# Kernel optimization log

Measured on AMD Instinct MI355X. Metric: run time of the kernel, lower is better.

Reference implementation:

```python
import jax, jax.numpy as jnp
import numpy as np

N, E, IN, H, C = 100_000, 1_600_000, 128, 4, 32  # nodes, edges, in_dim, heads, per-head channels
HC = H * C
SLOPE = 0.2  # negative_slope


def setup_inputs() -> dict:
    key = jax.random.key(0)
    ks = jax.random.split(key, 20)
    rn = lambda k, shape, s=0.05: jax.random.normal(k, shape, jnp.float32) * s
    inp = {
        'x': rn(ks[0], (N, IN), 1.0),
        'edge_index': jax.random.randint(ks[1], (2, E), 0, N),
    }
    for i in range(3):
        din = IN if i == 0 else HC
        inp[f'W{i}'] = rn(ks[2 + 4 * i], (din, HC))
        inp[f'as{i}'] = rn(ks[3 + 4 * i], (H, C))
        inp[f'ad{i}'] = rn(ks[4 + 4 * i], (H, C))
        inp[f'b{i}'] = jnp.zeros((HC,), jnp.float32)
    inp['llW'] = rn(ks[14], (HC, HC))
    inp['llb'] = jnp.zeros((HC,), jnp.float32)
    inp['opW'] = rn(ks[15], (3 * HC, C))  # concat_dim=384 -> out_dim=32
    inp['opb'] = jnp.zeros((C,), jnp.float32)
    return inp


def gat_layer(h, src, dst, W, a_s, a_d, b):
    # PyG GATConv with concat=True, add_self_loops=False, edge_dim=None, eval-mode dropout
    xh = (h @ W).reshape(-1, H, C)                        # [N,H,C]
    e_src = (xh * a_s).sum(-1)                            # [N,H]
    e_dst = (xh * a_d).sum(-1)                            # [N,H]
    e = jax.nn.leaky_relu(e_src[src] + e_dst[dst], SLOPE)  # [E,H]
    emax = jax.ops.segment_max(e, dst, num_segments=N)    # segment softmax over dst
    ee = jnp.exp(e - emax[dst])
    denom = jax.ops.segment_sum(ee, dst, num_segments=N)
    alpha = ee / denom[dst]                               # [E,H]
    out = jax.ops.segment_sum(xh[src] * alpha[:, :, None], dst, num_segments=N)  # [N,H,C]
    return out.reshape(-1, HC) + b


def reference(x, edge_index, W0, as0, ad0, b0, W1, as1, ad1, b1, W2, as2, ad2, b2, llW, llb, opW, opb):
    src, dst = edge_index[0], edge_index[1]
    # layer 0 (no residual at layer 0)
    h0 = gat_layer(x, src, dst, W0, as0, ad0, b0)
    # layer 1: residual
    h1 = gat_layer(h0, src, dst, W1, as1, ad1, b1) + h0
    # layer 2: residual through last_linear
    h2 = gat_layer(h1, src, dst, W2, as2, ad2, b2) + (h1 @ llW + llb)
    # encoder head: concat hidden list, project
    h = jnp.concatenate([h0, h1, h2], axis=-1)  # [N, 384]
    return h @ opW + opb                         # [N, 32]
```

## Files before the change

### kernel.cpp

```cpp
#include <hip/hip_runtime.h>
#include <hip/hip_bf16.h>

#define NN  100000
#define NE  1600000
#define NH4 400000
#define NHC 12800000
#define NBLK 391
#define SC_CHUNK 2048
#define SC_NCHUNK ((NE + SC_CHUNK - 1) / SC_CHUNK)

typedef __attribute__((ext_vector_type(8))) short bf16x8;
typedef __attribute__((ext_vector_type(4))) float f32x4;

__device__ __forceinline__ ushort f2bf(float f) {
  uint u = __float_as_uint(f);
  u += 0x7fff + ((u >> 16) & 1);
  return (ushort)(u >> 16);
}
__device__ __forceinline__ uint pack2(float a, float b) {
  return (uint)f2bf(a) | ((uint)f2bf(b) << 16);
}
__device__ __forceinline__ float blo(uint u) { return __uint_as_float(u << 16); }
__device__ __forceinline__ float bhi(uint u) { return __uint_as_float(u & 0xffff0000u); }

template <bool ABF16>
__global__ __launch_bounds__(256) void gemm128_k(const void* __restrict__ Av,
                                                 const float* __restrict__ W,
                                                 ushort* __restrict__ out,
                                                 const float* __restrict__ bias1,
                                                 const float* __restrict__ bias2) {
  __shared__ uint As[64 * 64];
  __shared__ uint Wt[128 * 64];
  const int tid = threadIdx.x;
  const int row0 = blockIdx.x * 64;

  if constexpr (ABF16) {
    const uint4* __restrict__ Ag = (const uint4*)((const uint*)Av + (size_t)row0 * 64);
#pragma unroll
    for (int i = 0; i < 4; i++) {
      const int idx = tid + 256 * i;
      const int r = idx >> 4, c4 = idx & 15;
      uint4 v = make_uint4(0u, 0u, 0u, 0u);
      if (row0 + r < NN) v = Ag[idx];
      const uint off = (uint)(r * 64 + c4 * 4) ^ (uint)((r & 7) << 2);
      *(uint4*)&As[off] = v;
    }
  } else {
    const float4* __restrict__ Ag = (const float4*)((const float*)Av + (size_t)row0 * 128);
#pragma unroll
    for (int i = 0; i < 8; i++) {
      const int idx = tid + 256 * i;
      const int r = idx >> 5, k4 = idx & 31;
      float4 a = make_float4(0.f, 0.f, 0.f, 0.f);
      if (row0 + r < NN) a = Ag[idx];
      uint2 p;
      p.x = pack2(a.x, a.y);
      p.y = pack2(a.z, a.w);
      const uint off = (uint)(r * 64 + k4 * 2) ^ (uint)((r & 7) << 2);
      *(uint2*)&As[off] = p;
    }
  }
  {
#pragma unroll
    for (int i = 0; i < 8; i++) {
      const int cid = tid + 256 * i;
      const int n = cid & 127;
      const int k8 = cid >> 7;
      float v[8];
#pragma unroll
      for (int j = 0; j < 8; j++) v[j] = W[(size_t)(k8 * 8 + j) * 128 + n];
      uint4 p;
      p.x = pack2(v[0], v[1]);
      p.y = pack2(v[2], v[3]);
      p.z = pack2(v[4], v[5]);
      p.w = pack2(v[6], v[7]);
      const uint off = (uint)(n * 64 + k8 * 4) ^ (uint)((n & 7) << 2);
      *(uint4*)&Wt[off] = p;
    }
  }
  __syncthreads();

  const int w = tid >> 6, l = tid & 63;
  const int lrow = l & 15;
  const int lku = (l >> 4) * 4;

  bf16x8 afrag[4];
#pragma unroll
  for (int kc = 0; kc < 4; kc++) {
    const int r = w * 16 + lrow;
    const uint off = (uint)(r * 64 + lku + kc * 16) ^ (uint)((r & 7) << 2);
    afrag[kc] = *(const bf16x8*)&As[off];
  }

#pragma unroll
  for (int nt = 0; nt < 8; nt++) {
    const int n = nt * 16 + lrow;
    f32x4 acc = {0.f, 0.f, 0.f, 0.f};
#pragma unroll
    for (int kc = 0; kc < 4; kc++) {
      const uint off = (uint)(n * 64 + lku + kc * 16) ^ (uint)((n & 7) << 2);
      const bf16x8 bfrag = *(const bf16x8*)&Wt[off];
      acc = __builtin_amdgcn_mfma_f32_16x16x32_bf16(afrag[kc], bfrag, acc, 0, 0, 0);
    }
    const int col = n;
    float badd = 0.f;
    if (bias1) badd += bias1[col];
    if (bias2) badd += bias2[col];
#pragma unroll
    for (int reg = 0; reg < 4; reg++) {
      const int r = row0 + w * 16 + (l >> 4) * 4 + reg;
      if (r < NN) out[(size_t)r * 128 + col] = f2bf(acc[reg] + badd);
    }
  }
}

__global__ __launch_bounds__(256) void attn_coef_k(const uint* __restrict__ xbf,
                                                   const float* __restrict__ as_,
                                                   const float* __restrict__ ad_,
                                                   float* __restrict__ es,
                                                   float* __restrict__ ed) {
  const int idx = blockIdx.x * 256 + threadIdx.x;
  if (idx >= NH4) return;
  const int h = idx & 3;
  const int ab = h * 32;
  const uint* row = xbf + (size_t)(idx >> 2) * 64 + h * 16;
  float s = 0.f, d = 0.f;
#pragma unroll
  for (int i = 0; i < 16; i += 4) {
    const uint4 v = *(const uint4*)(row + i);
#define UNP(u, k)                                                        \
    {                                                                    \
      const float lo = blo(u), hi = bhi(u);                              \
      s = fmaf(lo, as_[ab + (k)], fmaf(hi, as_[ab + (k) + 1], s));       \
      d = fmaf(lo, ad_[ab + (k)], fmaf(hi, ad_[ab + (k) + 1], d));       \
    }
    UNP(v.x, 2 * i) UNP(v.y, 2 * i + 2) UNP(v.z, 2 * i + 4) UNP(v.w, 2 * i + 6)
#undef UNP
  }
  es[idx] = s;
  ed[idx] = d;
}

__global__ __launch_bounds__(256) void hist_k(const int* __restrict__ dst, int* __restrict__ counts) {
  const int g = blockIdx.x & 7;
  const int chunk = blockIdx.x >> 3;
  const int lo = g * (NN / 8);
  const int hi = lo + (NN / 8);
  const int e0 = chunk * SC_CHUNK;
  const int e1 = (e0 + SC_CHUNK < NE) ? e0 + SC_CHUNK : NE;
  for (int i = e0 + threadIdx.x; i < e1; i += 256) {
    const int d = dst[i];
    if (d >= lo && d < hi) atomicAdd(&counts[d], 1);
  }
}

__global__ __launch_bounds__(256) void scan_blk_k(const int* __restrict__ counts,
                                                  int* __restrict__ row_start,
                                                  int* __restrict__ blocksum) {
  __shared__ int sm[256];
  const int t = threadIdx.x;
  const int i = blockIdx.x * 256 + t;
  const int c = (i < NN) ? counts[i] : 0;
  sm[t] = c;
  __syncthreads();
#pragma unroll
  for (int off = 1; off < 256; off <<= 1) {
    const int v = (t >= off) ? sm[t - off] : 0;
    __syncthreads();
    sm[t] += v;
    __syncthreads();
  }
  if (i < NN) row_start[i] = sm[t] - c;
  if (t == 255) blocksum[blockIdx.x] = sm[255];
}

__global__ __launch_bounds__(512) void scan_top_k(const int* __restrict__ blocksum,
                                                  int* __restrict__ blockoff) {
  __shared__ int sm[512];
  const int t = threadIdx.x;
  const int c = (t < NBLK) ? blocksum[t] : 0;
  sm[t] = c;
  __syncthreads();
#pragma unroll
  for (int off = 1; off < 512; off <<= 1) {
    const int v = (t >= off) ? sm[t - off] : 0;
    __syncthreads();
    sm[t] += v;
    __syncthreads();
  }
  if (t < NBLK) blockoff[t] = sm[t] - c;
}

__global__ __launch_bounds__(256) void scan_fix_k(int* __restrict__ row_start,
                                                  const int* __restrict__ blockoff,
                                                  int* __restrict__ cursor) {
  const int i = blockIdx.x * 256 + threadIdx.x;
  if (i < NN) {
    const int v = row_start[i] + blockoff[blockIdx.x];
    row_start[i] = v;
    cursor[i] = v;
  }
  if (i == 0) row_start[NN] = NE;
}

__global__ __launch_bounds__(256) void scatter_k(const int* __restrict__ src,
                                                 const int* __restrict__ dst,
                                                 int* __restrict__ cursor,
                                                 int* __restrict__ csr_src) {
  const int g = blockIdx.x & 7;
  const int chunk = blockIdx.x >> 3;
  const int lo = g * (NN / 8);
  const int hi = lo + (NN / 8);
  const int e0 = chunk * SC_CHUNK;
  const int e1 = (e0 + SC_CHUNK < NE) ? e0 + SC_CHUNK : NE;
  for (int i = e0 + threadIdx.x; i < e1; i += 256) {
    const int d = dst[i];
    if (d >= lo && d < hi) {
      const int pos = atomicAdd(&cursor[d], 1);
      csr_src[pos] = src[i];
    }
  }
}

#define EDGE_BODY(sv)                                                      \
  {                                                                        \
    const int s_ = (sv);                                                   \
    float v_ = es[s_ * 4 + h] + edh;                                       \
    v_ = v_ > 0.f ? v_ : 0.2f * v_;                                        \
    const float w_ = __expf(v_);                                           \
    const uint m_ = xbf[(size_t)s_ * 64 + l];                              \
    den += w_;                                                             \
    ax = fmaf(w_, blo(m_), ax);                                            \
    ay = fmaf(w_, bhi(m_), ay);                                            \
  }

__global__ __launch_bounds__(256) void gat_agg_k(const int* __restrict__ row_start,
                                                 const int* __restrict__ csr_src,
                                                 const float* __restrict__ es,
                                                 const float* __restrict__ ed,
                                                 const uint* __restrict__ xbf,
                                                 const ushort* __restrict__ base,
                                                 const float* __restrict__ bias,
                                                 ushort* __restrict__ out) {
  const int wid = (blockIdx.x * 256 + threadIdx.x) >> 6;
  if (wid >= NN) return;
  const int l = threadIdx.x & 63;
  const int h = l >> 4;
  const float edh = ed[wid * 4 + h];
  const int beg = row_start[wid], end = row_start[wid + 1];
  float ax = 0.f, ay = 0.f, den = 0.f;
  int i = beg;
  for (; i + 8 <= end; i += 8) {
    const int s0 = csr_src[i],     s1 = csr_src[i + 1];
    const int s2 = csr_src[i + 2], s3 = csr_src[i + 3];
    const int s4 = csr_src[i + 4], s5 = csr_src[i + 5];
    const int s6 = csr_src[i + 6], s7 = csr_src[i + 7];
    EDGE_BODY(s0) EDGE_BODY(s1) EDGE_BODY(s2) EDGE_BODY(s3)
    EDGE_BODY(s4) EDGE_BODY(s5) EDGE_BODY(s6) EDGE_BODY(s7)
  }
  for (; i + 4 <= end; i += 4) {
    const int s0 = csr_src[i],     s1 = csr_src[i + 1];
    const int s2 = csr_src[i + 2], s3 = csr_src[i + 3];
    EDGE_BODY(s0) EDGE_BODY(s1) EDGE_BODY(s2) EDGE_BODY(s3)
  }
  for (; i < end; i++) EDGE_BODY(csr_src[i]);

  const float inv = den > 0.f ? 1.f / den : 0.f;
  float rx = ax * inv, ry = ay * inv;
  const size_t o = (size_t)wid * 64 + l;
  if (base) {
    const uint b = ((const uint*)base)[o];
    rx += blo(b); ry += bhi(b);
  }
  if (bias) { rx += bias[l * 2]; ry += bias[l * 2 + 1]; }
  ((uint*)out)[o] = pack2(rx, ry);
}

__global__ __launch_bounds__(256) void out_proj_k(const ushort* __restrict__ h0,
                                                  const ushort* __restrict__ h1,
                                                  const ushort* __restrict__ h2,
                                                  const float* __restrict__ opW,
                                                  const float* __restrict__ opb,
                                                  float* __restrict__ out) {
  const int cb = __builtin_amdgcn_readfirstlane((threadIdx.x >> 6) * 8);
  const int l = threadIdx.x & 63;
  const int n = blockIdx.x * 64 + l;
  if (n >= NN) return;

  float acc[8];
#pragma unroll
  for (int j = 0; j < 8; j++) acc[j] = opb[cb + j];

  const uint4* __restrict__ rp[3] = {
      (const uint4*)((const uint*)h0 + (size_t)n * 64),
      (const uint4*)((const uint*)h1 + (size_t)n * 64),
      (const uint4*)((const uint*)h2 + (size_t)n * 64)};

#pragma unroll
  for (int seg = 0; seg < 3; seg++) {
    const uint4* __restrict__ r = rp[seg];
    for (int k8 = 0; k8 < 16; k8++) {
      const uint4 v = r[k8];
      float av[8];
      av[0] = blo(v.x); av[1] = bhi(v.x);
      av[2] = blo(v.y); av[3] = bhi(v.y);
      av[4] = blo(v.z); av[5] = bhi(v.z);
      av[6] = blo(v.w); av[7] = bhi(v.w);
      const float* __restrict__ wr = opW + (size_t)(seg * 128 + k8 * 8) * 32 + cb;
#pragma unroll
      for (int q = 0; q < 8; q++)
#pragma unroll
        for (int j = 0; j < 8; j++)
          acc[j] = fmaf(av[q], wr[q * 32 + j], acc[j]);
    }
  }

  float* __restrict__ o = out + (size_t)n * 32 + cb;
  *(float4*)(o + 0) = make_float4(acc[0], acc[1], acc[2], acc[3]);
  *(float4*)(o + 4) = make_float4(acc[4], acc[5], acc[6], acc[7]);
}

extern "C" void kernel_launch(void* const* d_in, const int* in_sizes, int n_in,
                              void* d_out, int out_size, void* d_ws, size_t ws_size,
                              hipStream_t stream) {
  (void)in_sizes; (void)n_in; (void)out_size; (void)ws_size;
  const float* x  = (const float*)d_in[0];
  const int*   ei = (const int*)d_in[1];
  const int*  src = ei;
  const int*  dst = ei + NE;
  const float *W0 = (const float*)d_in[2],  *as0 = (const float*)d_in[3],
              *ad0 = (const float*)d_in[4], *b0 = (const float*)d_in[5];
  const float *W1 = (const float*)d_in[6],  *as1 = (const float*)d_in[7],
              *ad1 = (const float*)d_in[8], *b1 = (const float*)d_in[9];
  const float *W2 = (const float*)d_in[10], *as2 = (const float*)d_in[11],
              *ad2 = (const float*)d_in[12], *b2 = (const float*)d_in[13];
  const float *llW = (const float*)d_in[14], *llb = (const float*)d_in[15];
  const float *opW = (const float*)d_in[16], *opb = (const float*)d_in[17];

  char* w = (char*)d_ws;
  ushort* h0b = (ushort*)w; w += (size_t)NHC * 2;
  ushort* h1b = (ushort*)w; w += (size_t)NHC * 2;
  ushort* h2b = (ushort*)w; w += (size_t)NHC * 2;
  uint*   xbf = (uint*)w;   w += (size_t)NHC * 2;
  float*  es  = (float*)w;  w += (size_t)NH4 * 4;
  float*  ed  = (float*)w;  w += (size_t)NH4 * 4;
  int* row_start = (int*)w; w += (size_t)(NN + 1) * 4;
  int* cursor    = (int*)w; w += (size_t)NN * 4;
  int* counts    = (int*)w; w += (size_t)NN * 4;
  int* csr_src   = (int*)w; w += (size_t)NE * 4;
  int* blocksum  = (int*)w; w += (size_t)NBLK * 4;
  int* blockoff  = (int*)w;

  const dim3 blk(256);
  hipMemsetAsync(counts, 0, (size_t)NN * 4, stream);
  hist_k<<<SC_NCHUNK * 8, blk, 0, stream>>>(dst, counts);
  scan_blk_k<<<NBLK, blk, 0, stream>>>(counts, row_start, blocksum);
  scan_top_k<<<1, 512, 0, stream>>>(blocksum, blockoff);
  scan_fix_k<<<NBLK, blk, 0, stream>>>(row_start, blockoff, cursor);
  scatter_k<<<SC_NCHUNK * 8, blk, 0, stream>>>(src, dst, cursor, csr_src);
  gemm128_k<false><<<1563, blk, 0, stream>>>(x, W0, (ushort*)xbf, nullptr, nullptr);
  attn_coef_k<<<1563, blk, 0, stream>>>(xbf, as0, ad0, es, ed);
  gat_agg_k<<<25000, blk, 0, stream>>>(row_start, csr_src, es, ed, xbf, nullptr, b0, h0b);
  gemm128_k<true><<<1563, blk, 0, stream>>>(h0b, W1, (ushort*)xbf, nullptr, nullptr);
  attn_coef_k<<<1563, blk, 0, stream>>>(xbf, as1, ad1, es, ed);
  gat_agg_k<<<25000, blk, 0, stream>>>(row_start, csr_src, es, ed, xbf, h0b, b1, h1b);
  gemm128_k<true><<<1563, blk, 0, stream>>>(h1b, llW, h2b, llb, b2);
  gemm128_k<true><<<1563, blk, 0, stream>>>(h1b, W2, (ushort*)xbf, nullptr, nullptr);
  attn_coef_k<<<1563, blk, 0, stream>>>(xbf, as2, ad2, es, ed);
  gat_agg_k<<<25000, blk, 0, stream>>>(row_start, csr_src, es, ed, xbf, h2b, nullptr, h2b);
  out_proj_k<<<1563, blk, 0, stream>>>(h0b, h1b, h2b, opW, opb, (float*)d_out);
}
```

Measured before the change: 582.3 us.

## Precompute per-edge attention weights and enlarge GEMM row tile to 128

```diff
diff --git a/kernel.cpp b/kernel.cpp
--- a/kernel.cpp
+++ b/kernel.cpp
@@ -24,21 +24,21 @@
 __device__ __forceinline__ float bhi(uint u) { return __uint_as_float(u & 0xffff0000u); }
 
 template <bool ABF16>
-__global__ __launch_bounds__(256) void gemm128_k(const void* __restrict__ Av,
+__global__ __launch_bounds__(512) void gemm128_k(const void* __restrict__ Av,
                                                  const float* __restrict__ W,
                                                  ushort* __restrict__ out,
                                                  const float* __restrict__ bias1,
                                                  const float* __restrict__ bias2) {
-  __shared__ uint As[64 * 64];
+  __shared__ uint As[128 * 64];
   __shared__ uint Wt[128 * 64];
   const int tid = threadIdx.x;
-  const int row0 = blockIdx.x * 64;
+  const int row0 = blockIdx.x * 128;
 
   if constexpr (ABF16) {
     const uint4* __restrict__ Ag = (const uint4*)((const uint*)Av + (size_t)row0 * 64);
 #pragma unroll
     for (int i = 0; i < 4; i++) {
-      const int idx = tid + 256 * i;
+      const int idx = tid + 512 * i;
       const int r = idx >> 4, c4 = idx & 15;
       uint4 v = make_uint4(0u, 0u, 0u, 0u);
       if (row0 + r < NN) v = Ag[idx];
@@ -49,7 +49,7 @@
     const float4* __restrict__ Ag = (const float4*)((const float*)Av + (size_t)row0 * 128);
 #pragma unroll
     for (int i = 0; i < 8; i++) {
-      const int idx = tid + 256 * i;
+      const int idx = tid + 512 * i;
       const int r = idx >> 5, k4 = idx & 31;
       float4 a = make_float4(0.f, 0.f, 0.f, 0.f);
       if (row0 + r < NN) a = Ag[idx];
@@ -62,8 +62,8 @@
   }
   {
 #pragma unroll
-    for (int i = 0; i < 8; i++) {
-      const int cid = tid + 256 * i;
+    for (int i = 0; i < 4; i++) {
+      const int cid = tid + 512 * i;
       const int n = cid & 127;
       const int k8 = cid >> 7;
       float v[8];
@@ -206,7 +206,8 @@
 __global__ __launch_bounds__(256) void scatter_k(const int* __restrict__ src,
                                                  const int* __restrict__ dst,
                                                  int* __restrict__ cursor,
-                                                 int* __restrict__ csr_src) {
+                                                 int* __restrict__ csr_src,
+                                                 int* __restrict__ csr_dst) {
   const int g = blockIdx.x & 7;
   const int chunk = blockIdx.x >> 3;
   const int lo = g * (NN / 8);
@@ -218,26 +219,28 @@
     if (d >= lo && d < hi) {
       const int pos = atomicAdd(&cursor[d], 1);
       csr_src[pos] = src[i];
-    }
-  }
-}
-
-#define EDGE_BODY(sv)                                                      \
-  {                                                                        \
-    const int s_ = (sv);                                                   \
-    float v_ = es[s_ * 4 + h] + edh;                                       \
-    v_ = v_ > 0.f ? v_ : 0.2f * v_;                                        \
-    const float w_ = __expf(v_);                                           \
-    const uint m_ = xbf[(size_t)s_ * 64 + l];                              \
-    den += w_;                                                             \
-    ax = fmaf(w_, blo(m_), ax);                                            \
-    ay = fmaf(w_, bhi(m_), ay);                                            \
-  }
+      csr_dst[pos] = d;
+    }
+  }
+}
+
+__global__ __launch_bounds__(256) void edge_w_k(const int* __restrict__ csr_src,
+                                                const int* __restrict__ csr_dst,
+                                                const float* __restrict__ es,
+                                                const float* __restrict__ ed,
+                                                float* __restrict__ csr_w) {
+  const int idx = blockIdx.x * 256 + threadIdx.x;
+  const int j = idx >> 2, h = idx & 3;
+  if (j >= NE) return;
+  const int s = csr_src[j], d = csr_dst[j];
+  float v = es[s * 4 + h] + ed[d * 4 + h];
+  v = v > 0.f ? v : 0.2f * v;
+  csr_w[idx] = __expf(v);
+}
 
 __global__ __launch_bounds__(256) void gat_agg_k(const int* __restrict__ row_start,
                                                  const int* __restrict__ csr_src,
-                                                 const float* __restrict__ es,
-                                                 const float* __restrict__ ed,
+                                                 const float* __restrict__ csr_w,
                                                  const uint* __restrict__ xbf,
                                                  const ushort* __restrict__ base,
                                                  const float* __restrict__ bias,
@@ -246,24 +249,32 @@
   if (wid >= NN) return;
   const int l = threadIdx.x & 63;
   const int h = l >> 4;
-  const float edh = ed[wid * 4 + h];
   const int beg = row_start[wid], end = row_start[wid + 1];
   float ax = 0.f, ay = 0.f, den = 0.f;
   int i = beg;
   for (; i + 8 <= end; i += 8) {
-    const int s0 = csr_src[i],     s1 = csr_src[i + 1];
-    const int s2 = csr_src[i + 2], s3 = csr_src[i + 3];
-    const int s4 = csr_src[i + 4], s5 = csr_src[i + 5];
-    const int s6 = csr_src[i + 6], s7 = csr_src[i + 7];
-    EDGE_BODY(s0) EDGE_BODY(s1) EDGE_BODY(s2) EDGE_BODY(s3)
-    EDGE_BODY(s4) EDGE_BODY(s5) EDGE_BODY(s6) EDGE_BODY(s7)
-  }
-  for (; i + 4 <= end; i += 4) {
-    const int s0 = csr_src[i],     s1 = csr_src[i + 1];
-    const int s2 = csr_src[i + 2], s3 = csr_src[i + 3];
-    EDGE_BODY(s0) EDGE_BODY(s1) EDGE_BODY(s2) EDGE_BODY(s3)
-  }
-  for (; i < end; i++) EDGE_BODY(csr_src[i]);
+    int s[8]; float wv[8]; uint m[8];
+#pragma unroll
+    for (int q = 0; q < 8; q++) s[q] = csr_src[i + q];
+#pragma unroll
+    for (int q = 0; q < 8; q++) wv[q] = csr_w[(size_t)(i + q) * 4 + h];
+#pragma unroll
+    for (int q = 0; q < 8; q++) m[q] = xbf[(size_t)s[q] * 64 + l];
+#pragma unroll
+    for (int q = 0; q < 8; q++) {
+      den += wv[q];
+      ax = fmaf(wv[q], blo(m[q]), ax);
+      ay = fmaf(wv[q], bhi(m[q]), ay);
+    }
+  }
+  for (; i < end; i++) {
+    const int s_ = csr_src[i];
+    const float w_ = csr_w[(size_t)i * 4 + h];
+    const uint m_ = xbf[(size_t)s_ * 64 + l];
+    den += w_;
+    ax = fmaf(w_, blo(m_), ax);
+    ay = fmaf(w_, bhi(m_), ay);
+  }
 
   const float inv = den > 0.f ? 1.f / den : 0.f;
   float rx = ax * inv, ry = ay * inv;
@@ -344,10 +355,12 @@
   uint*   xbf = (uint*)w;   w += (size_t)NHC * 2;
   float*  es  = (float*)w;  w += (size_t)NH4 * 4;
   float*  ed  = (float*)w;  w += (size_t)NH4 * 4;
+  float*  csr_w = (float*)w; w += (size_t)NE * 4 * 4;
   int* row_start = (int*)w; w += (size_t)(NN + 1) * 4;
   int* cursor    = (int*)w; w += (size_t)NN * 4;
   int* counts    = (int*)w; w += (size_t)NN * 4;
   int* csr_src   = (int*)w; w += (size_t)NE * 4;
+  int* csr_dst   = (int*)w; w += (size_t)NE * 4;
   int* blocksum  = (int*)w; w += (size_t)NBLK * 4;
   int* blockoff  = (int*)w;
 
@@ -357,16 +370,19 @@
   scan_blk_k<<<NBLK, blk, 0, stream>>>(counts, row_start, blocksum);
   scan_top_k<<<1, 512, 0, stream>>>(blocksum, blockoff);
   scan_fix_k<<<NBLK, blk, 0, stream>>>(row_start, blockoff, cursor);
-  scatter_k<<<SC_NCHUNK * 8, blk, 0, stream>>>(src, dst, cursor, csr_src);
-  gemm128_k<false><<<1563, blk, 0, stream>>>(x, W0, (ushort*)xbf, nullptr, nullptr);
+  scatter_k<<<SC_NCHUNK * 8, blk, 0, stream>>>(src, dst, cursor, csr_src, csr_dst);
+  gemm128_k<false><<<782, 512, 0, stream>>>(x, W0, (ushort*)xbf, nullptr, nullptr);
   attn_coef_k<<<1563, blk, 0, stream>>>(xbf, as0, ad0, es, ed);
-  gat_agg_k<<<25000, blk, 0, stream>>>(row_start, csr_src, es, ed, xbf, nullptr, b0, h0b);
-  gemm128_k<true><<<1563, blk, 0, stream>>>(h0b, W1, (ushort*)xbf, nullptr, nullptr);
+  edge_w_k<<<25000, blk, 0, stream>>>(csr_src, csr_dst, es, ed, csr_w);
+  gat_agg_k<<<25000, blk, 0, stream>>>(row_start, csr_src, csr_w, xbf, nullptr, b0, h0b);
+  gemm128_k<true><<<782, 512, 0, stream>>>(h0b, W1, (ushort*)xbf, nullptr, nullptr);
   attn_coef_k<<<1563, blk, 0, stream>>>(xbf, as1, ad1, es, ed);
-  gat_agg_k<<<25000, blk, 0, stream>>>(row_start, csr_src, es, ed, xbf, h0b, b1, h1b);
-  gemm128_k<true><<<1563, blk, 0, stream>>>(h1b, llW, h2b, llb, b2);
-  gemm128_k<true><<<1563, blk, 0, stream>>>(h1b, W2, (ushort*)xbf, nullptr, nullptr);
+  edge_w_k<<<25000, blk, 0, stream>>>(csr_src, csr_dst, es, ed, csr_w);
+  gat_agg_k<<<25000, blk, 0, stream>>>(row_start, csr_src, csr_w, xbf, h0b, b1, h1b);
+  gemm128_k<true><<<782, 512, 0, stream>>>(h1b, llW, h2b, llb, b2);
+  gemm128_k<true><<<782, 512, 0, stream>>>(h1b, W2, (ushort*)xbf, nullptr, nullptr);
   attn_coef_k<<<1563, blk, 0, stream>>>(xbf, as2, ad2, es, ed);
-  gat_agg_k<<<25000, blk, 0, stream>>>(row_start, csr_src, es, ed, xbf, h2b, nullptr, h2b);
+  edge_w_k<<<25000, blk, 0, stream>>>(csr_src, csr_dst, es, ed, csr_w);
+  gat_agg_k<<<25000, blk, 0, stream>>>(row_start, csr_src, csr_w, xbf, h2b, nullptr, h2b);
   out_proj_k<<<1563, blk, 0, stream>>>(h0b, h1b, h2b, opW, opb, (float*)d_out);
 }
```

New measurement: 624.8 us. +7.3%, slower.
